# Kernel tuning notes

Hardware: AMD Instinct MI355X
Metric: run time of the kernel (lower is better)

## Reference

```python
import jax, jax.numpy as jnp
import numpy as np

MODES = 16  # FourierLayer default


def _fourier_layer(h, w):
    # h: [B, S, H] real; w: [H, H, MODES] complex
    S = h.shape[1]
    h_ft = jnp.fft.rfft(h, axis=1)                 # [B, F, H] complex, F = S//2+1
    m = min(MODES, h_ft.shape[1])
    # batched complex matmul over the retained low-frequency modes
    out_m = jnp.einsum('bmh,hkm->bmk', h_ft[:, :m, :], w[:, :, :m])
    out_ft = jnp.zeros_like(h_ft).at[:, :m, :].set(out_m)  # higher modes zeroed
    h = jnp.fft.irfft(out_ft, n=S, axis=1)
    return jax.nn.gelu(h, approximate=False)       # torch nn.GELU() is exact erf


def setup_inputs() -> dict:
    key = jax.random.key(0)
    ks = jax.random.split(key, 7)
    B, S, H, L = 32, 8192, 128, 4
    x = jax.random.normal(ks[0], (B, S), jnp.float32)
    proj_w = jax.random.normal(ks[1], (H,), jnp.float32)          # Linear(1,H).weight[:,0]
    proj_b = jax.random.normal(ks[2], (H,), jnp.float32) * 0.02
    w_re = jax.random.normal(ks[3], (L, H, H, MODES), jnp.float32) * 0.02
    w_im = jax.random.normal(ks[4], (L, H, H, MODES), jnp.float32) * 0.02
    out_w = jax.random.normal(ks[5], (H,), jnp.float32) * 0.02    # Linear(H,1).weight[0]
    out_b = jax.random.normal(ks[6], (1,), jnp.float32) * 0.02
    return {"x": x, "proj_w": proj_w, "proj_b": proj_b,
            "w_re": w_re, "w_im": w_im, "out_w": out_w, "out_b": out_b}


def reference(x, proj_w, proj_b, w_re, w_im, out_w, out_b):
    # projection: Linear(1, H) applied to x.unsqueeze(-1)
    h = x[..., None] * proj_w + proj_b            # [B, S, H]
    W = (w_re + 1j * w_im).astype(jnp.complex64)  # [L, H, H, MODES]
    for l in range(w_re.shape[0]):                # fixed small layer count
        h = _fourier_layer(h, W[l])
    # output projection Linear(H, 1) then squeeze(-1)
    return h @ out_w + out_b[0]                   # [B, S]
```

## Files before the change

kernel.cpp:

```cpp
#include <hip/hip_runtime.h>
#include <hip/hip_bf16.h>

#define S_LEN 8192
#define NH 128
#define NM 16
#define NB 32
#define NBATCH 32

typedef __hip_bfloat16 bf16;
typedef unsigned short ushort_t;
typedef unsigned int uint_t;

typedef __bf16 bf16x8 __attribute__((ext_vector_type(8)));
typedef float floatx4 __attribute__((ext_vector_type(4)));

__device__ __forceinline__ float b2f(bf16 v){ return __bfloat162float(v); }
__device__ __forceinline__ float ldf(const void* p, long i, int f32){
    return f32 ? ((const float*)p)[i] : b2f(((const bf16*)p)[i]);
}
__device__ __forceinline__ float gelu_fast(float x){
    float z = fabsf(x) * 0.70710678118654752440f;
    float t = __builtin_amdgcn_rcpf(__builtin_fmaf(0.3275911f, z, 1.0f));
    float p = t*(0.254829592f + t*(-0.284496736f + t*(1.421413741f +
              t*(-1.453152027f + t*1.061405429f))));
    float e = __expf(-z * z);
    float er = __builtin_fmaf(-p, e, 1.0f);
    float s = copysignf(er, x);
    return 0.5f * x * (1.0f + s);
}
__device__ __forceinline__ ushort_t f2us(float v){
    return __builtin_bit_cast(ushort_t, (__bf16)v);
}
__device__ __forceinline__ void split_bf(float v, ushort_t& hi, ushort_t& lo){
    __bf16 h = (__bf16)v;
    float r = v - (float)h;
    hi = __builtin_bit_cast(ushort_t, h);
    lo = __builtin_bit_cast(ushort_t, (__bf16)r);
}
__device__ __forceinline__ bf16x8 ld8(const ushort_t* p){
    return *(const bf16x8*)(const void*)p;
}
__device__ __forceinline__ floatx4 MF(bf16x8 a, bf16x8 b, floatx4 c){
    return __builtin_amdgcn_mfma_f32_16x16x32_bf16(a, b, c, 0, 0, 0);
}

__device__ __forceinline__ int detect_f32(const void* x, int tid){
    __shared__ int sflag;
    if (tid < 64){
        const ushort_t* p = (const ushort_t*)x;
        int cnt = 0;
        for (int i = tid; i < 4096; i += 64){
            int e = (p[i] >> 7) & 0xFF;
            if (e >= 0xA0) cnt++;
        }
        #pragma unroll
        for (int off = 32; off > 0; off >>= 1) cnt += __shfl_xor(cnt, off, 64);
        if (tid == 0) sflag = (cnt > 400) ? 1 : 0;
    }
    __syncthreads();
    return sflag;
}

__device__ __forceinline__ void c_prologue(const float* __restrict__ C,
                                           int b, int c, int q,
                                           bf16x8* Bhi, bf16x8* Blo){
    const float* Cb = C + (long)b * NB * NH;
    #pragma unroll
    for (int kt = 0; kt < 8; kt++){
        int k = kt * 16 + c;
        bf16x8 h8, l8;
        #pragma unroll
        for (int e = 0; e < 8; e++){
            int j = 8 * q + e;
            float sc = (j == 0) ? (1.0f / S_LEN)
                     : (j < NM) ? (2.0f / S_LEN)
                     : (j == NM) ? 0.f : (-2.0f / S_LEN);
            float v = Cb[j * NH + k] * sc;
            __bf16 hh = (__bf16)v;
            h8[e] = hh;
            l8[e] = (__bf16)(v - (float)hh);
        }
        Bhi[kt] = h8; Blo[kt] = l8;
    }
}

__global__ __launch_bounds__(256) void k_prep(const void* __restrict__ x,
                                              const void* __restrict__ pw,
                                              const void* __restrict__ pb,
                                              float* __restrict__ M,
                                              ushort_t* __restrict__ Thi,
                                              ushort_t* __restrict__ Tlo,
                                              ushort_t* __restrict__ TThi,
                                              float* __restrict__ C0){
    int bid = blockIdx.x;
    int tid = threadIdx.x;
    int f32 = detect_f32(x, tid);
    if (bid < 512){
        int m = bid >> 5, b = bid & 31;
        float re = 0.f, im = 0.f;
        #pragma unroll 4
        for (int s = tid; s < S_LEN; s += 256){
            float xv = ldf(x, (long)b * S_LEN + s, f32);
            if (m){
                int r = (m * s) & (S_LEN - 1);
                float rev = (float)r * (1.0f / (float)S_LEN);
                float sv = __builtin_amdgcn_sinf(rev);
                float cv = __builtin_amdgcn_cosf(rev);
                re += xv * cv;
                im -= xv * sv;
            } else {
                re += xv;
            }
        }
        __shared__ float sred[8];
        #pragma unroll
        for (int off = 32; off > 0; off >>= 1){
            re += __shfl_xor(re, off, 64);
            im += __shfl_xor(im, off, 64);
        }
        int w = tid >> 6;
        if ((tid & 63) == 0){ sred[w] = re; sred[4 + w] = im; }
        __syncthreads();
        if (tid < NH){
            float Xre = sred[0] + sred[1] + sred[2] + sred[3];
            float Xim = sred[4] + sred[5] + sred[6] + sred[7];
            int h = tid;
            float pwv = ldf(pw, h, f32);
            float fc = pwv * Xre + (m == 0 ? (float)S_LEN * ldf(pb, h, f32) : 0.f);
            float fs = -pwv * Xim;
            float* Mb = M + (long)b * NB * NH;
            Mb[m * NH + h]        = fc;
            Mb[(NM + m) * NH + h] = fs;
        }
    } else {
        int bb = bid - 512;
        int s = bb * 16 + (tid >> 4);
        int m = tid & 15;
        float cv = 1.f, sv = 0.f;
        if (m){
            int r = (m * s) & (S_LEN - 1);
            float rev = (float)r * (1.0f / (float)S_LEN);
            sv = __builtin_amdgcn_sinf(rev);
            cv = __builtin_amdgcn_cosf(rev);
        }
        ushort_t chi, clo, shi, slo;
        split_bf(cv, chi, clo);
        split_bf(sv, shi, slo);
        Thi[s * NB + m] = chi;       Tlo[s * NB + m] = clo;
        Thi[s * NB + NM + m] = shi;  Tlo[s * NB + NM + m] = slo;
        TThi[m * S_LEN + s] = chi;
        TThi[(NM + m) * S_LEN + s] = shi;
        C0[bb * 256 + tid] = 0.f;
    }
}

__global__ __launch_bounds__(256) void k_mixA(const void* __restrict__ x,
                                              const float* __restrict__ M,
                                              const void* __restrict__ wre,
                                              const void* __restrict__ wim,
                                              long woff,
                                              float* __restrict__ C){
    int tid = threadIdx.x;
    int f32 = detect_f32(x, tid);
    int hc = blockIdx.x, b = blockIdx.y;
    int k = tid & 127, mh = tid >> 7;
    int m0 = mh * 8;
    int h0 = hc * 16;
    __shared__ float Ms[NB * 16];
    for (int i = tid; i < NB * 16; i += 256){
        int j = i >> 4, hh = i & 15;
        Ms[j * 16 + hh] = M[(long)b * NB * NH + j * NH + h0 + hh];
    }
    __syncthreads();
    float Cr[8] = {0,0,0,0,0,0,0,0}, Ci[8] = {0,0,0,0,0,0,0,0};
    #pragma unroll 4
    for (int hh = 0; hh < 16; hh++){
        long base = woff + ((long)(h0 + hh) * NH + k) * NM + m0;
        float wr[8], wi[8];
        if (f32){
            const float4* wr4 = (const float4*)((const float*)wre + base);
            const float4* wi4 = (const float4*)((const float*)wim + base);
            float4 a0 = wr4[0], a1 = wr4[1], c0 = wi4[0], c1 = wi4[1];
            wr[0]=a0.x; wr[1]=a0.y; wr[2]=a0.z; wr[3]=a0.w;
            wr[4]=a1.x; wr[5]=a1.y; wr[6]=a1.z; wr[7]=a1.w;
            wi[0]=c0.x; wi[1]=c0.y; wi[2]=c0.z; wi[3]=c0.w;
            wi[4]=c1.x; wi[5]=c1.y; wi[6]=c1.z; wi[7]=c1.w;
        } else {
            bf16x8 a = ld8((const ushort_t*)wre + base);
            bf16x8 c = ld8((const ushort_t*)wim + base);
            #pragma unroll
            for (int e = 0; e < 8; e++){ wr[e] = (float)a[e]; wi[e] = (float)c[e]; }
        }
        #pragma unroll
        for (int e = 0; e < 8; e++){
            float fc = Ms[(m0 + e) * 16 + hh];
            float fs = Ms[(NM + m0 + e) * 16 + hh];
            Cr[e] += fc * wr[e] + fs * wi[e];
            Ci[e] += fc * wi[e] - fs * wr[e];
        }
    }
    float* Cb = C + (long)b * NB * NH;
    #pragma unroll
    for (int e = 0; e < 8; e++){
        atomicAdd(&Cb[(m0 + e) * NH + k],      Cr[e]);
        atomicAdd(&Cb[(NM + m0 + e) * NH + k], Ci[e]);
    }
}

__global__ __launch_bounds__(256) void k_reduce(const float* __restrict__ Mpart,
                                                float* __restrict__ Mfull){
    int r = blockIdx.x, b = blockIdx.y;
    int idx = r * 256 + threadIdx.x;
    const float* mp = Mpart + (long)b * 32 * (NB * NH) + idx;
    float acc = 0.f;
    #pragma unroll
    for (int sx = 0; sx < 32; sx++) acc += mp[(long)sx * (NB * NH)];
    Mfull[(long)b * (NB * NH) + idx] = acc;
}

__global__ __launch_bounds__(256, 4) void k_fused2(const ushort_t* __restrict__ Thi,
                                                   const ushort_t* __restrict__ Tlo,
                                                   const ushort_t* __restrict__ TThi,
                                                   const float* __restrict__ C,
                                                   float* __restrict__ Cnext,
                                                   float* __restrict__ Mpart){
    int b = blockIdx.y;
    int sx = blockIdx.x;
    int tid = threadIdx.x;
    int w = tid >> 6;
    int lane = tid & 63;
    int c = lane & 15, q = lane >> 4;
    int kt0 = 2 * w;
    __shared__ __align__(16) ushort_t G[4][32][40];

    bf16x8 Bhi[2], Blo[2];
    {
        const float* Cb = C + (long)b * NB * NH;
        #pragma unroll
        for (int ktl = 0; ktl < 2; ktl++){
            int k = (kt0 + ktl) * 16 + c;
            bf16x8 h8, l8;
            #pragma unroll
            for (int e = 0; e < 8; e++){
                int j = 8 * q + e;
                float sc = (j == 0) ? (1.0f / S_LEN)
                         : (j < NM) ? (2.0f / S_LEN)
                         : (j == NM) ? 0.f : (-2.0f / S_LEN);
                float v = Cb[j * NH + k] * sc;
                __bf16 hh = (__bf16)v;
                h8[e] = hh;
                l8[e] = (__bf16)(v - (float)hh);
            }
            Bhi[ktl] = h8; Blo[ktl] = l8;
        }
    }
    if (tid < 32){
        *(float4*)(Cnext + (long)b * NB * NH + sx * 128 + tid * 4)
            = (float4){0.f, 0.f, 0.f, 0.f};
    }

    floatx4 a00 = {0,0,0,0}, a01 = {0,0,0,0}, a10 = {0,0,0,0}, a11 = {0,0,0,0};
    int s0B = sx * 256;
    #pragma unroll 2
    for (int t2 = 0; t2 < 8; t2++){
        int sc0 = s0B + 32 * t2;
        bf16x8 Ahi[2], Alo[2];
        #pragma unroll
        for (int tt = 0; tt < 2; tt++){
            long ar = (long)(sc0 + 16 * tt + c) * NB + 8 * q;
            Ahi[tt] = ld8(Thi + ar);
            Alo[tt] = ld8(Tlo + ar);
        }
        bf16x8 Att0 = ld8(TThi + (long)c * S_LEN + sc0 + 8 * q);
        bf16x8 Att1 = ld8(TThi + (long)(16 + c) * S_LEN + sc0 + 8 * q);
        #pragma unroll
        for (int tt = 0; tt < 2; tt++){
            #pragma unroll
            for (int ktl = 0; ktl < 2; ktl++){
                floatx4 acc = {0.f, 0.f, 0.f, 0.f};
                acc = MF(Ahi[tt], Bhi[ktl], acc);
                acc = MF(Alo[tt], Bhi[ktl], acc);
                acc = MF(Ahi[tt], Blo[ktl], acc);
                uint_t u0 = (uint_t)f2us(gelu_fast(acc[0])) |
                            ((uint_t)f2us(gelu_fast(acc[1])) << 16);
                uint_t u1 = (uint_t)f2us(gelu_fast(acc[2])) |
                            ((uint_t)f2us(gelu_fast(acc[3])) << 16);
                uint2 uu; uu.x = u0; uu.y = u1;
                *(uint2*)(void*)&G[w][16 * ktl + c][16 * tt + 4 * q] = uu;
            }
        }
        bf16x8 P0 = *(const bf16x8*)(const void*)&G[w][c][8 * q];
        bf16x8 P1 = *(const bf16x8*)(const void*)&G[w][16 + c][8 * q];
        a00 = MF(Att0, P0, a00);
        a01 = MF(Att0, P1, a01);
        a10 = MF(Att1, P0, a10);
        a11 = MF(Att1, P1, a11);
    }
    float* Mb = Mpart + ((long)b * 32 + sx) * (NB * NH);
    #pragma unroll
    for (int r = 0; r < 4; r++){
        Mb[(4 * q + r) * NH + kt0 * 16 + c]            = a00[r];
        Mb[(4 * q + r) * NH + (kt0 + 1) * 16 + c]      = a01[r];
        Mb[(16 + 4 * q + r) * NH + kt0 * 16 + c]       = a10[r];
        Mb[(16 + 4 * q + r) * NH + (kt0 + 1) * 16 + c] = a11[r];
    }
}

__global__ __launch_bounds__(256) void k_final(const void* __restrict__ x,
                                               const ushort_t* __restrict__ Thi,
                                               const ushort_t* __restrict__ Tlo,
                                               const float* __restrict__ C,
                                               const void* __restrict__ ow,
                                               const void* __restrict__ ob,
                                               void* __restrict__ out){
    int tid = threadIdx.x;
    int f32 = detect_f32(x, tid);
    int b = blockIdx.y;
    int s0 = blockIdx.x * 128;
    int w = tid >> 6;
    int lane = tid & 63;
    int c = lane & 15, q = lane >> 4;

    bf16x8 Bhi[8], Blo[8];
    c_prologue(C, b, c, q, Bhi, Blo);
    float ow8[8];
    #pragma unroll
    for (int kt = 0; kt < 8; kt++) ow8[kt] = ldf(ow, kt * 16 + c, f32);
    float obv = ldf(ob, 0, f32);
    #pragma unroll
    for (int sti = 0; sti < 2; sti++){
        int st = w * 2 + sti;
        long ar = (long)(s0 + st * 16 + c) * NB + 8 * q;
        bf16x8 Ahi = ld8(Thi + ar);
        bf16x8 Alo = ld8(Tlo + ar);
        float p0 = 0.f, p1 = 0.f, p2 = 0.f, p3 = 0.f;
        #pragma unroll
        for (int g = 0; g < 2; g++){
            int k0 = g * 4;
            floatx4 ac[4];
            #pragma unroll
            for (int t = 0; t < 4; t++) ac[t] = (floatx4){0.f, 0.f, 0.f, 0.f};
            #pragma unroll
            for (int t = 0; t < 4; t++) ac[t] = MF(Ahi, Bhi[k0 + t], ac[t]);
            #pragma unroll
            for (int t = 0; t < 4; t++) ac[t] = MF(Alo, Bhi[k0 + t], ac[t]);
            #pragma unroll
            for (int t = 0; t < 4; t++) ac[t] = MF(Ahi, Blo[k0 + t], ac[t]);
            #pragma unroll
            for (int t = 0; t < 4; t++){
                float o = ow8[k0 + t];
                p0 += gelu_fast(ac[t][0]) * o;
                p1 += gelu_fast(ac[t][1]) * o;
                p2 += gelu_fast(ac[t][2]) * o;
                p3 += gelu_fast(ac[t][3]) * o;
            }
        }
        #pragma unroll
        for (int off = 1; off < 16; off <<= 1){
            p0 += __shfl_xor(p0, off, 16);
            p1 += __shfl_xor(p1, off, 16);
            p2 += __shfl_xor(p2, off, 16);
            p3 += __shfl_xor(p3, off, 16);
        }
        if (c == 0){
            long s = s0 + st * 16 + 4 * q;
            if (f32){
                float4 v = {p0 + obv, p1 + obv, p2 + obv, p3 + obv};
                *(float4*)((float*)out + (long)b * S_LEN + s) = v;
            } else {
                uint_t u0 = (uint_t)f2us(p0 + obv) | ((uint_t)f2us(p1 + obv) << 16);
                uint_t u1 = (uint_t)f2us(p2 + obv) | ((uint_t)f2us(p3 + obv) << 16);
                uint_t* gp = (uint_t*)((ushort_t*)out + (long)b * S_LEN + s);
                gp[0] = u0; gp[1] = u1;
            }
        }
    }
}

extern "C" void kernel_launch(void* const* d_in, const int* in_sizes, int n_in,
                              void* d_out, int out_size, void* d_ws, size_t ws_size,
                              hipStream_t stream) {
    const void* x   = d_in[0];
    const void* pw  = d_in[1];
    const void* pb  = d_in[2];
    const void* wre = d_in[3];
    const void* wim = d_in[4];
    const void* ow  = d_in[5];
    const void* ob  = d_in[6];

    char* ws = (char*)d_ws;
    ushort_t* Thi  = (ushort_t*)(ws);
    ushort_t* Tlo  = (ushort_t*)(ws + (512u << 10));
    ushort_t* TThi = (ushort_t*)(ws + (1024u << 10));
    float* C0    = (float*)(ws + (1536u << 10));
    float* C1    = (float*)(ws + (2048u << 10));
    float* Mfull = (float*)(ws + (2560u << 10));
    float* Mpart = (float*)(ws + (3072u << 10));

    const long wstride = (long)NH * NH * NM;

    k_prep<<<1024, 256, 0, stream>>>(x, pw, pb, Mfull, Thi, Tlo, TThi, C0);
    k_mixA<<<dim3(8, NBATCH), 256, 0, stream>>>(x, Mfull, wre, wim,
                                                0 * wstride, C0);
    k_fused2<<<dim3(32, NBATCH), 256, 0, stream>>>(Thi, Tlo, TThi, C0, C1, Mpart);
    k_reduce<<<dim3(16, NBATCH), 256, 0, stream>>>(Mpart, Mfull);
    k_mixA<<<dim3(8, NBATCH), 256, 0, stream>>>(x, Mfull, wre, wim,
                                                1 * wstride, C1);
    k_fused2<<<dim3(32, NBATCH), 256, 0, stream>>>(Thi, Tlo, TThi, C1, C0, Mpart);
    k_reduce<<<dim3(16, NBATCH), 256, 0, stream>>>(Mpart, Mfull);
    k_mixA<<<dim3(8, NBATCH), 256, 0, stream>>>(x, Mfull, wre, wim,
                                                2 * wstride, C0);
    k_fused2<<<dim3(32, NBATCH), 256, 0, stream>>>(Thi, Tlo, TThi, C0, C1, Mpart);
    k_reduce<<<dim3(16, NBATCH), 256, 0, stream>>>(Mpart, Mfull);
    k_mixA<<<dim3(8, NBATCH), 256, 0, stream>>>(x, Mfull, wre, wim,
                                                3 * wstride, C1);
    k_final<<<dim3(64, NBATCH), 256, 0, stream>>>(x, Thi, Tlo, C1, ow, ob, d_out);
}
```

Before: 251.1 us.

## Replace atomic mode-mix accumulation with partial buffers and split work across more blocks

k_mixA now splits the modes over an extra grid dimension, so each block handles 4 modes instead of 8. It writes per-h-chunk partial sums to a buffer instead of using float atomics, and a new k_redC kernel reduces them. That also removes the need to zero C in k_prep and k_fused2. k_fused2 doubles its grid to 64 s-chunks of 128 with a 64-way reduction afterwards, and the launch bounds raise the occupancy targets. The aim is more parallelism and fewer atomic contention stalls, at the cost of four extra small kernel launches and more partial-buffer traffic.

```diff
diff --git a/kernel.cpp b/kernel.cpp
--- a/kernel.cpp
+++ b/kernel.cpp
@@ -90,8 +90,7 @@
                                               float* __restrict__ M,
                                               ushort_t* __restrict__ Thi,
                                               ushort_t* __restrict__ Tlo,
-                                              ushort_t* __restrict__ TThi,
-                                              float* __restrict__ C0){
+                                              ushort_t* __restrict__ TThi){
     int bid = blockIdx.x;
     int tid = threadIdx.x;
     int f32 = detect_f32(x, tid);
@@ -150,21 +149,20 @@
         Thi[s * NB + NM + m] = shi;  Tlo[s * NB + NM + m] = slo;
         TThi[m * S_LEN + s] = chi;
         TThi[(NM + m) * S_LEN + s] = shi;
-        C0[bb * 256 + tid] = 0.f;
-    }
-}
-
-__global__ __launch_bounds__(256) void k_mixA(const void* __restrict__ x,
-                                              const float* __restrict__ M,
-                                              const void* __restrict__ wre,
-                                              const void* __restrict__ wim,
-                                              long woff,
-                                              float* __restrict__ C){
+    }
+}
+
+__global__ __launch_bounds__(256, 6) void k_mixA(const void* __restrict__ x,
+                                                 const float* __restrict__ M,
+                                                 const void* __restrict__ wre,
+                                                 const void* __restrict__ wim,
+                                                 long woff,
+                                                 float* __restrict__ Cpart){
     int tid = threadIdx.x;
     int f32 = detect_f32(x, tid);
-    int hc = blockIdx.x, b = blockIdx.y;
-    int k = tid & 127, mh = tid >> 7;
-    int m0 = mh * 8;
+    int hc = blockIdx.x, mg = blockIdx.y, b = blockIdx.z;
+    int k = tid & 127, msub = tid >> 7;
+    int m0 = mg * 8 + msub * 4;
     int h0 = hc * 16;
     __shared__ float Ms[NB * 16];
     for (int i = tid; i < NB * 16; i += 256){
@@ -172,57 +170,70 @@
         Ms[j * 16 + hh] = M[(long)b * NB * NH + j * NH + h0 + hh];
     }
     __syncthreads();
-    float Cr[8] = {0,0,0,0,0,0,0,0}, Ci[8] = {0,0,0,0,0,0,0,0};
+    float Cr[4] = {0,0,0,0}, Ci[4] = {0,0,0,0};
     #pragma unroll 4
     for (int hh = 0; hh < 16; hh++){
         long base = woff + ((long)(h0 + hh) * NH + k) * NM + m0;
-        float wr[8], wi[8];
+        float wr[4], wi[4];
         if (f32){
-            const float4* wr4 = (const float4*)((const float*)wre + base);
-            const float4* wi4 = (const float4*)((const float*)wim + base);
-            float4 a0 = wr4[0], a1 = wr4[1], c0 = wi4[0], c1 = wi4[1];
-            wr[0]=a0.x; wr[1]=a0.y; wr[2]=a0.z; wr[3]=a0.w;
-            wr[4]=a1.x; wr[5]=a1.y; wr[6]=a1.z; wr[7]=a1.w;
-            wi[0]=c0.x; wi[1]=c0.y; wi[2]=c0.z; wi[3]=c0.w;
-            wi[4]=c1.x; wi[5]=c1.y; wi[6]=c1.z; wi[7]=c1.w;
+            float4 a  = *(const float4*)((const float*)wre + base);
+            float4 cc = *(const float4*)((const float*)wim + base);
+            wr[0]=a.x;  wr[1]=a.y;  wr[2]=a.z;  wr[3]=a.w;
+            wi[0]=cc.x; wi[1]=cc.y; wi[2]=cc.z; wi[3]=cc.w;
         } else {
-            bf16x8 a = ld8((const ushort_t*)wre + base);
-            bf16x8 c = ld8((const ushort_t*)wim + base);
-            #pragma unroll
-            for (int e = 0; e < 8; e++){ wr[e] = (float)a[e]; wi[e] = (float)c[e]; }
-        }
-        #pragma unroll
-        for (int e = 0; e < 8; e++){
+            ushort4 a  = *(const ushort4*)((const ushort_t*)wre + base);
+            ushort4 cc = *(const ushort4*)((const ushort_t*)wim + base);
+            wr[0]=b2f(__builtin_bit_cast(bf16, a.x));
+            wr[1]=b2f(__builtin_bit_cast(bf16, a.y));
+            wr[2]=b2f(__builtin_bit_cast(bf16, a.z));
+            wr[3]=b2f(__builtin_bit_cast(bf16, a.w));
+            wi[0]=b2f(__builtin_bit_cast(bf16, cc.x));
+            wi[1]=b2f(__builtin_bit_cast(bf16, cc.y));
+            wi[2]=b2f(__builtin_bit_cast(bf16, cc.z));
+            wi[3]=b2f(__builtin_bit_cast(bf16, cc.w));
+        }
+        #pragma unroll
+        for (int e = 0; e < 4; e++){
             float fc = Ms[(m0 + e) * 16 + hh];
             float fs = Ms[(NM + m0 + e) * 16 + hh];
             Cr[e] += fc * wr[e] + fs * wi[e];
             Ci[e] += fc * wi[e] - fs * wr[e];
         }
     }
-    float* Cb = C + (long)b * NB * NH;
-    #pragma unroll
-    for (int e = 0; e < 8; e++){
-        atomicAdd(&Cb[(m0 + e) * NH + k],      Cr[e]);
-        atomicAdd(&Cb[(NM + m0 + e) * NH + k], Ci[e]);
-    }
-}
-
-__global__ __launch_bounds__(256) void k_reduce(const float* __restrict__ Mpart,
-                                                float* __restrict__ Mfull){
+    float* Cb = Cpart + ((long)hc * NBATCH + b) * (NB * NH);
+    #pragma unroll
+    for (int e = 0; e < 4; e++){
+        Cb[(m0 + e) * NH + k]        = Cr[e];
+        Cb[(NM + m0 + e) * NH + k]   = Ci[e];
+    }
+}
+
+__global__ __launch_bounds__(256, 8) void k_redC(const float* __restrict__ Cpart,
+                                                 float* __restrict__ C){
+    int r = blockIdx.x, b = blockIdx.y;
+    int i = r * 256 + threadIdx.x;
+    const float* cp = Cpart + (long)b * (NB * NH) + i;
+    float acc = 0.f;
+    #pragma unroll
+    for (int hc = 0; hc < 8; hc++) acc += cp[(long)hc * NBATCH * (NB * NH)];
+    C[(long)b * (NB * NH) + i] = acc;
+}
+
+__global__ __launch_bounds__(256, 8) void k_redM(const float* __restrict__ Mpart,
+                                                 float* __restrict__ Mfull){
     int r = blockIdx.x, b = blockIdx.y;
     int idx = r * 256 + threadIdx.x;
-    const float* mp = Mpart + (long)b * 32 * (NB * NH) + idx;
+    const float* mp = Mpart + (long)b * 64 * (NB * NH) + idx;
     float acc = 0.f;
-    #pragma unroll
-    for (int sx = 0; sx < 32; sx++) acc += mp[(long)sx * (NB * NH)];
+    #pragma unroll 16
+    for (int sx = 0; sx < 64; sx++) acc += mp[(long)sx * (NB * NH)];
     Mfull[(long)b * (NB * NH) + idx] = acc;
 }
 
-__global__ __launch_bounds__(256, 4) void k_fused2(const ushort_t* __restrict__ Thi,
+__global__ __launch_bounds__(256, 6) void k_fused2(const ushort_t* __restrict__ Thi,
                                                    const ushort_t* __restrict__ Tlo,
                                                    const ushort_t* __restrict__ TThi,
                                                    const float* __restrict__ C,
-                                                   float* __restrict__ Cnext,
                                                    float* __restrict__ Mpart){
     int b = blockIdx.y;
     int sx = blockIdx.x;
@@ -254,15 +265,11 @@
             Bhi[ktl] = h8; Blo[ktl] = l8;
         }
     }
-    if (tid < 32){
-        *(float4*)(Cnext + (long)b * NB * NH + sx * 128 + tid * 4)
-            = (float4){0.f, 0.f, 0.f, 0.f};
-    }
 
     floatx4 a00 = {0,0,0,0}, a01 = {0,0,0,0}, a10 = {0,0,0,0}, a11 = {0,0,0,0};
-    int s0B = sx * 256;
+    int s0B = sx * 128;
     #pragma unroll 2
-    for (int t2 = 0; t2 < 8; t2++){
+    for (int t2 = 0; t2 < 4; t2++){
         int sc0 = s0B + 32 * t2;
         bf16x8 Ahi[2], Alo[2];
         #pragma unroll
@@ -296,7 +303,7 @@
         a10 = MF(Att1, P0, a10);
         a11 = MF(Att1, P1, a11);
     }
-    float* Mb = Mpart + ((long)b * 32 + sx) * (NB * NH);
+    float* Mb = Mpart + ((long)b * 64 + sx) * (NB * NH);
     #pragma unroll
     for (int r = 0; r < 4; r++){
         Mb[(4 * q + r) * NH + kt0 * 16 + c]            = a00[r];
@@ -306,13 +313,13 @@
     }
 }
 
-__global__ __launch_bounds__(256) void k_final(const void* __restrict__ x,
-                                               const ushort_t* __restrict__ Thi,
-                                               const ushort_t* __restrict__ Tlo,
-                                               const float* __restrict__ C,
-                                               const void* __restrict__ ow,
-                                               const void* __restrict__ ob,
-                                               void* __restrict__ out){
+__global__ __launch_bounds__(256, 4) void k_final(const void* __restrict__ x,
+                                                  const ushort_t* __restrict__ Thi,
+                                                  const ushort_t* __restrict__ Tlo,
+                                                  const float* __restrict__ C,
+                                                  const void* __restrict__ ow,
+                                                  const void* __restrict__ ob,
+                                                  void* __restrict__ out){
     int tid = threadIdx.x;
     int f32 = detect_f32(x, tid);
     int b = blockIdx.y;
@@ -392,27 +399,25 @@
     ushort_t* Thi  = (ushort_t*)(ws);
     ushort_t* Tlo  = (ushort_t*)(ws + (512u << 10));
     ushort_t* TThi = (ushort_t*)(ws + (1024u << 10));
-    float* C0    = (float*)(ws + (1536u << 10));
-    float* C1    = (float*)(ws + (2048u << 10));
-    float* Mfull = (float*)(ws + (2560u << 10));
-    float* Mpart = (float*)(ws + (3072u << 10));
+    float* C     = (float*)(ws + (1536u << 10));
+    float* Mfull = (float*)(ws + (2048u << 10));
+    float* Cpart = (float*)(ws + (2560u << 10));
+    float* Mpart = (float*)(ws + (6656u << 10));
 
     const long wstride = (long)NH * NH * NM;
 
-    k_prep<<<1024, 256, 0, stream>>>(x, pw, pb, Mfull, Thi, Tlo, TThi, C0);
-    k_mixA<<<dim3(8, NBATCH), 256, 0, stream>>>(x, Mfull, wre, wim,
-                                                0 * wstride, C0);
-    k_fused2<<<dim3(32, NBATCH), 256, 0, stream>>>(Thi, Tlo, TThi, C0, C1, Mpart);
-    k_reduce<<<dim3(16, NBATCH), 256, 0, stream>>>(Mpart, Mfull);
-    k_mixA<<<dim3(8, NBATCH), 256, 0, stream>>>(x, Mfull, wre, wim,
-                                                1 * wstride, C1);
-    k_fused2<<<dim3(32, NBATCH), 256, 0, stream>>>(Thi, Tlo, TThi, C1, C0, Mpart);
-    k_reduce<<<dim3(16, NBATCH), 256, 0, stream>>>(Mpart, Mfull);
-    k_mixA<<<dim3(8, NBATCH), 256, 0, stream>>>(x, Mfull, wre, wim,
-                                                2 * wstride, C0);
-    k_fused2<<<dim3(32, NBATCH), 256, 0, stream>>>(Thi, Tlo, TThi, C0, C1, Mpart);
-    k_reduce<<<dim3(16, NBATCH), 256, 0, stream>>>(Mpart, Mfull);
-    k_mixA<<<dim3(8, NBATCH), 256, 0, stream>>>(x, Mfull, wre, wim,
-                                                3 * wstride, C1);
-    k_final<<<dim3(64, NBATCH), 256, 0, stream>>>(x, Thi, Tlo, C1, ow, ob, d_out);
-}
+    k_prep<<<1024, 256, 0, stream>>>(x, pw, pb, Mfull, Thi, Tlo, TThi);
+    for (int l = 0; l < 4; l++){
+        k_mixA<<<dim3(8, 2, NBATCH), 256, 0, stream>>>(x, Mfull, wre, wim,
+                                                       l * wstride, Cpart);
+        k_redC<<<dim3(4, NBATCH), 256, 0, stream>>>(Cpart, C);
+        if (l < 3){
+            k_fused2<<<dim3(64, NBATCH), 256, 0, stream>>>(Thi, Tlo, TThi,
+                                                           C, Mpart);
+            k_redM<<<dim3(16, NBATCH), 256, 0, stream>>>(Mpart, Mfull);
+        } else {
+            k_final<<<dim3(64, NBATCH), 256, 0, stream>>>(x, Thi, Tlo, C,
+                                                          ow, ob, d_out);
+        }
+    }
+}
```

Measured after the change: 283.1 us. 1.13x slower.
